# Kernel tuning notes

Measured on AMD Instinct MI355X. Metric: run time of the kernel, lower is better.

## Reference

```python
import jax, jax.numpy as jnp
import numpy as np

PI = 3.141592653589793
N = 4194304


def _lerp(a, b, w):
    return a + w * (b - a)


def _schlick(u):
    m = jnp.clip(1.0 - u, 0.0, 1.0)
    return m ** 5


def setup_inputs() -> dict:
    key = jax.random.key(0)
    kl, kv, kp = jax.random.split(key, 3)

    def unit_dirs(k):
        v = jax.random.normal(k, (N, 3), dtype=jnp.float32)
        v = v / jnp.linalg.norm(v, axis=-1, keepdims=True)
        # upper hemisphere so most samples pass the cos_nl/cos_nv >= 0 test
        return v.at[:, 2].set(jnp.abs(v[:, 2]))

    light = unit_dirs(kl)
    view = unit_dirs(kv)
    inputs = jnp.stack([light, view], axis=1)  # [N, 2, 3]

    return {
        "inputs": inputs,
        "base_color": jnp.array([0.8, 0.8, 0.8], dtype=jnp.float32),
        "metallic": jnp.array([0.3], dtype=jnp.float32),
        "subsurface": jnp.array([0.2], dtype=jnp.float32),
        "specular": jnp.array([0.5], dtype=jnp.float32),
        "roughness": jnp.array([0.5], dtype=jnp.float32),
        "specular_tint": jnp.array([0.1], dtype=jnp.float32),
        "anisotropic": jnp.array([0.2], dtype=jnp.float32),
        "sheen": jnp.array([0.3], dtype=jnp.float32),
        "sheen_tint": jnp.array([0.5], dtype=jnp.float32),
        "clear_coat": jnp.array([0.5], dtype=jnp.float32),
        "clear_coat_gloss": jnp.array([0.8], dtype=jnp.float32),
    }


def _brdf(inputs, base_color, metallic, subsurface, specular, roughness,
          specular_tint, anisotropic, sheen, sheen_tint, clear_coat,
          clear_coat_gloss):
    # scalar params
    mtl = metallic[0]; sub = subsurface[0]; spec = specular[0]
    rough = roughness[0]; sp_tint = specular_tint[0]; aniso = anisotropic[0]
    sh = sheen[0]; sh_tint = sheen_tint[0]; cc = clear_coat[0]
    cc_gloss = clear_coat_gloss[0]

    light = inputs[:, 0, :]  # [N, 3]
    view = inputs[:, 1, :]   # [N, 3]
    hv = light + view
    half = hv / jnp.linalg.norm(hv, axis=-1, keepdims=True)

    # tangent x=[1,0,0], bitangent y=[0,1,0], normal=[0,0,1]
    cos_nl = light[:, 2]
    cos_nv = view[:, 2]
    cos_nh = half[:, 2]
    cos_hl = jnp.sum(half * light, axis=-1)

    valid = (cos_nl >= 0) & (cos_nv >= 0)
    # grad-safe cosines for invalid (masked-out) samples
    cnl = jnp.where(valid, cos_nl, 0.5)
    cnv = jnp.where(valid, cos_nv, 0.5)

    cd_lin = base_color ** 2.2  # mon2lin
    cd_lum = 0.3 * cd_lin[0] + 0.6 * cd_lin[1] + 0.1 * cd_lin[2]
    c_tint = jnp.where(cd_lum > 0, cd_lin / jnp.maximum(cd_lum, 1e-20),
                       jnp.zeros(3, cd_lin.dtype))

    c_spec0 = _lerp(spec * 0.08 * _lerp(1.0, c_tint, sp_tint), cd_lin, mtl)  # [3]
    c_sheen = _lerp(1.0, c_tint, sh_tint)  # [3]

    fl = _schlick(cnl)
    fv = _schlick(cnv)
    fd90 = 0.5 + 2.0 * cos_hl ** 2 * rough
    fd = _lerp(1.0, fd90, fl) * _lerp(1.0, fd90, fv)
    fss90 = cos_hl ** 2 * rough
    fss = _lerp(1.0, fss90, fl) * _lerp(1.0, fss90, fv)
    ss = 1.25 * (fss * (1.0 / (cnl + cnv) - 0.5) + 0.5)

    aspect = jnp.sqrt(1.0 - aniso * 0.9)
    ax = jnp.maximum(0.001, rough ** 2 / aspect)
    ay = jnp.maximum(0.001, rough ** 2 * aspect)

    # GTR2 anisotropic distribution
    Ds = 1.0 / (PI * ax * ay * ((half[:, 0] / ax) ** 2 +
                                (half[:, 1] / ay) ** 2 + cos_nh ** 2) ** 2)
    FH = _schlick(cos_hl)
    Fs = _lerp(c_spec0[None, :], 1.0, FH[:, None])  # [N, 3]

    def g_aniso(c, cx, cy):
        return 1.0 / (c + jnp.sqrt((cx * ax) ** 2 + (cy * ay) ** 2 + c ** 2))

    Gs = g_aniso(cnl, light[:, 0], light[:, 1]) * g_aniso(cnv, view[:, 0], view[:, 1])
    specular_term = (Gs * Ds)[:, None] * Fs

    Fsheen = FH[:, None] * sh * c_sheen[None, :]
    diffuse = ((1.0 / PI) * _lerp(fd, ss, sub)[:, None] * cd_lin[None, :] +
               Fsheen) * (1.0 - mtl)

    # clearcoat: GTR1 with a = lerp(0.1, 0.001, gloss)
    a_cc = _lerp(0.1, 0.001, cc_gloss)
    a2 = a_cc ** 2
    t = 1.0 + (a2 - 1.0) * cos_nh ** 2
    Dr = jnp.where(a_cc >= 1.0, 1.0 / PI, (a2 - 1.0) / (PI * jnp.log(a2) * t))

    def g025(c):
        a = 0.0625  # 0.25^2
        return 1.0 / (c + jnp.sqrt(a + c ** 2 - a * c ** 2))

    Gr = g025(cnl) * g025(cnv)
    Fr = _lerp(0.04, 1.0, FH)
    clear = 0.25 * cc * Gr * Fr * Dr

    out = diffuse + specular_term + clear[:, None]
    return jnp.where(valid[:, None], out, 0.0)


@jax.jit
def reference(inputs, base_color, metallic, subsurface, specular, roughness,
              specular_tint, anisotropic, sheen, sheen_tint, clear_coat,
              clear_coat_gloss):
    return _brdf(inputs, base_color, metallic, subsurface, specular, roughness,
                 specular_tint, anisotropic, sheen, sheen_tint, clear_coat,
                 clear_coat_gloss)
```

## Files before the change

### kernel.cpp

```cpp
#include <hip/hip_runtime.h>

#define PI_F 3.14159265358979323846f
#define THREADS 256
#define PTS_PER_BLOCK 512

__device__ __forceinline__ float rcpf_(float x){ return __builtin_amdgcn_rcpf(x); }
__device__ __forceinline__ float sqrtf_(float x){ return __builtin_amdgcn_sqrtf(x); }

__device__ __forceinline__ float schlick5(float u){
    float m = 1.0f - u;
    float m2 = m * m;
    return m2 * m2 * m;
}

__device__ __forceinline__ void compute_uniforms(
    const float* bc, float mtl, float sub, float spec, float rough,
    float sp_tint, float aniso, float sh, float sh_tint, float cc, float ccg,
    float* u)
{
    const float cd0 = __powf(bc[0], 2.2f);
    const float cd1 = __powf(bc[1], 2.2f);
    const float cd2 = __powf(bc[2], 2.2f);
    const float lum = 0.3f*cd0 + 0.6f*cd1 + 0.1f*cd2;
    const float il  = rcpf_(fmaxf(lum, 1e-20f));
    const float ct0 = (lum > 0.f) ? cd0*il : 0.f;
    const float ct1 = (lum > 0.f) ? cd1*il : 0.f;
    const float ct2 = (lum > 0.f) ? cd2*il : 0.f;

    const float s008 = spec * 0.08f;
    const float b0 = s008 * (1.f + sp_tint*(ct0 - 1.f));
    const float b1 = s008 * (1.f + sp_tint*(ct1 - 1.f));
    const float b2 = s008 * (1.f + sp_tint*(ct2 - 1.f));
    const float cs0_0 = b0 + mtl*(cd0 - b0);
    const float cs0_1 = b1 + mtl*(cd1 - b1);
    const float cs0_2 = b2 + mtl*(cd2 - b2);

    const float om = 1.f - mtl;
    const float invpi = 1.f / PI_F;

    const float aspect = sqrtf_(1.f - aniso*0.9f);
    const float r2 = rough * rough;
    const float ax = fmaxf(0.001f, r2 * rcpf_(aspect));
    const float ay = fmaxf(0.001f, r2 * aspect);

    const float a_cc = 0.1f + (0.001f - 0.1f)*ccg;
    const float a2 = a_cc * a_cc;
    float a2m1, k_dr;
    if (a_cc >= 1.0f) { a2m1 = 0.f; k_dr = invpi; }
    else              { a2m1 = a2 - 1.f; k_dr = (a2 - 1.f) * rcpf_(PI_F * __logf(a2)); }

    u[0] = rough;
    u[1] = sub;
    u[2] = ax*ax;
    u[3] = ay*ay;
    u[4] = rcpf_(ax*ax);
    u[5] = rcpf_(ay*ay);
    u[6] = rcpf_(PI_F * ax * ay);
    u[7] = a2m1;
    u[8] = k_dr;
    u[9] = 0.25f * cc;
    u[10] = cd0 * om * invpi;
    u[11] = cd1 * om * invpi;
    u[12] = cd2 * om * invpi;
    u[13] = sh * (1.f + sh_tint*(ct0 - 1.f)) * om;
    u[14] = sh * (1.f + sh_tint*(ct1 - 1.f)) * om;
    u[15] = sh * (1.f + sh_tint*(ct2 - 1.f)) * om;
    u[16] = cs0_0;
    u[17] = cs0_1;
    u[18] = cs0_2;
    u[19] = 1.f - cs0_0;
    u[20] = 1.f - cs0_1;
    u[21] = 1.f - cs0_2;
}

__global__ void setup_kernel(
    const float* __restrict__ bc, const float* __restrict__ metallic,
    const float* __restrict__ subsurface, const float* __restrict__ specular,
    const float* __restrict__ roughness, const float* __restrict__ specular_tint,
    const float* __restrict__ anisotropic, const float* __restrict__ sheen,
    const float* __restrict__ sheen_tint, const float* __restrict__ clear_coat,
    const float* __restrict__ clear_coat_gloss, float* __restrict__ ws)
{
    if (threadIdx.x == 0) {
        float u[22];
        compute_uniforms(bc, metallic[0], subsurface[0], specular[0], roughness[0],
                         specular_tint[0], anisotropic[0], sheen[0], sheen_tint[0],
                         clear_coat[0], clear_coat_gloss[0], u);
        #pragma unroll
        for (int i = 0; i < 22; ++i) ws[i] = u[i];
    }
}

__global__ __launch_bounds__(THREADS, 4) void brdf_kernel(
    const float* __restrict__ in,
    const float* __restrict__ uws,
    float* __restrict__ out,
    int npts)
{
    __shared__ float4 s_in4[PTS_PER_BLOCK * 6 / 4];
    __shared__ float2 s_out2[PTS_PER_BLOCK * 3 / 2];
    float* s_in = reinterpret_cast<float*>(s_in4);
    float* s_out = reinterpret_cast<float*>(s_out2);

    float U[22];
    #pragma unroll
    for (int i = 0; i < 22; ++i) U[i] = uws[i];
    const float rough   = U[0],  sub     = U[1];
    const float ax2     = U[2],  ay2     = U[3];
    const float inv_ax2 = U[4],  inv_ay2 = U[5];
    const float k_ds    = U[6],  a2m1    = U[7];
    const float k_dr    = U[8],  cc_q    = U[9];
    const float two_rough = 2.f * rough;

    const int j = threadIdx.x;
    const size_t blk = blockIdx.x;

    const size_t total_f4 = (size_t)npts * 6 / 4;
    const float4* gin = reinterpret_cast<const float4*>(in);
    const size_t f4_base = blk * (PTS_PER_BLOCK * 6 / 4);
    #pragma unroll
    for (int k = 0; k < 3; ++k) {
        size_t idx = f4_base + j + k * THREADS;
        if (idx < total_f4) s_in4[j + k * THREADS] = gin[idx];
    }
    __syncthreads();

    #pragma unroll
    for (int k = 0; k < 2; ++k) {
        const int p = j + k * THREADS;
        const float l0 = s_in[6*p+0], l1 = s_in[6*p+1], l2 = s_in[6*p+2];
        const float v0 = s_in[6*p+3], v1 = s_in[6*p+4], v2 = s_in[6*p+5];

        const float hvx = l0 + v0, hvy = l1 + v1, hvz = l2 + v2;
        const float n2 = hvx*hvx + hvy*hvy + hvz*hvz;
        const float chl = 0.5f * sqrtf_(n2);
        const float chl2 = 0.25f * n2;

        const bool valid = (l2 >= 0.f) && (v2 >= 0.f);
        const float cnl = valid ? l2 : 0.5f;
        const float cnv = valid ? v2 : 0.5f;

        const float fl = schlick5(cnl);
        const float fv = schlick5(cnv);
        const float FH = schlick5(chl);

        const float fd90m1  = two_rough * chl2 - 0.5f;
        const float fd  = (1.f + fd90m1*fl) * (1.f + fd90m1*fv);
        const float fss90m1 = rough * chl2 - 1.f;
        const float fss = (1.f + fss90m1*fl) * (1.f + fss90m1*fv);
        const float ss = 1.25f * (fss * (rcpf_(cnl + cnv) - 0.5f) + 0.5f);
        const float dw = fd + sub * (ss - fd);

        const float dtermu = hvx*hvx*inv_ax2 + hvy*hvy*inv_ay2 + hvz*hvz;
        const float denL = cnl + sqrtf_(l0*l0*ax2 + l1*l1*ay2 + cnl*cnl);
        const float denV = cnv + sqrtf_(v0*v0*ax2 + v1*v1*ay2 + cnv*cnv);
        const float GsDs = k_ds * (n2 * n2) * rcpf_(dtermu*dtermu * denL * denV);

        const float tden = n2 + a2m1 * (hvz*hvz);
        const float grL = cnl + sqrtf_(0.0625f + 0.9375f*cnl*cnl);
        const float grV = cnv + sqrtf_(0.0625f + 0.9375f*cnv*cnv);
        const float Fr = 0.04f + 0.96f * FH;
        const float clear = cc_q * Fr * k_dr * n2 * rcpf_(tden * grL * grV);

        float r0 = dw*U[10] + FH*U[13] + GsDs*(U[16] + FH*U[19]) + clear;
        float r1 = dw*U[11] + FH*U[14] + GsDs*(U[17] + FH*U[20]) + clear;
        float r2 = dw*U[12] + FH*U[15] + GsDs*(U[18] + FH*U[21]) + clear;

        s_out[3*p+0] = valid ? r0 : 0.f;
        s_out[3*p+1] = valid ? r1 : 0.f;
        s_out[3*p+2] = valid ? r2 : 0.f;
    }
    __syncthreads();

    const size_t total_f2 = (size_t)npts * 3 / 2;
    float2* gout = reinterpret_cast<float2*>(out);
    const size_t f2_base = blk * (PTS_PER_BLOCK * 3 / 2);
    #pragma unroll
    for (int k = 0; k < 3; ++k) {
        size_t idx = f2_base + j + k * THREADS;
        if (idx < total_f2) gout[idx] = s_out2[j + k * THREADS];
    }
}

extern "C" void kernel_launch(void* const* d_in, const int* in_sizes, int n_in,
                              void* d_out, int out_size, void* d_ws, size_t ws_size,
                              hipStream_t stream) {
    const float* in = (const float*)d_in[0];
    const int npts = in_sizes[0] / 6;
    const int grid = (npts + PTS_PER_BLOCK - 1) / PTS_PER_BLOCK;

    float* ws = (float*)d_ws;
    setup_kernel<<<1, 64, 0, stream>>>(
        (const float*)d_in[1], (const float*)d_in[2], (const float*)d_in[3],
        (const float*)d_in[4], (const float*)d_in[5], (const float*)d_in[6],
        (const float*)d_in[7], (const float*)d_in[8], (const float*)d_in[9],
        (const float*)d_in[10], (const float*)d_in[11], ws);

    brdf_kernel<<<grid, THREADS, 0, stream>>>(in, ws, (float*)d_out, npts);
}
```

Before: 181.7 us.

## Use persistent grid-stride blocks with register prefetch of next tile

Replaces one-block-per-tile launch with a capped persistent grid of 1536 blocks that loop over tiles. Each iteration issues global loads for the next tile into registers before computing the current tile, so load latency overlaps compute. This cuts block launch overhead and keeps memory requests in flight, but adds register pressure (12 extra floats) and may lower occupancy under the existing launch bounds.

Result: slower. 186.3 us (+2.5%).

```diff
diff --git a/kernel.cpp b/kernel.cpp
--- a/kernel.cpp
+++ b/kernel.cpp
@@ -3,6 +3,9 @@
 #define PI_F 3.14159265358979323846f
 #define THREADS 256
 #define PTS_PER_BLOCK 512
+#define F4_PER_TILE (PTS_PER_BLOCK * 6 / 4)
+#define F2_PER_TILE (PTS_PER_BLOCK * 3 / 2)
+#define PERSIST_BLOCKS 1536
 
 __device__ __forceinline__ float rcpf_(float x){ return __builtin_amdgcn_rcpf(x); }
 __device__ __forceinline__ float sqrtf_(float x){ return __builtin_amdgcn_sqrtf(x); }
@@ -95,10 +98,10 @@
     const float* __restrict__ in,
     const float* __restrict__ uws,
     float* __restrict__ out,
-    int npts)
+    int npts, int ntiles)
 {
-    __shared__ float4 s_in4[PTS_PER_BLOCK * 6 / 4];
-    __shared__ float2 s_out2[PTS_PER_BLOCK * 3 / 2];
+    __shared__ float4 s_in4[F4_PER_TILE];
+    __shared__ float2 s_out2[F2_PER_TILE];
     float* s_in = reinterpret_cast<float*>(s_in4);
     float* s_out = reinterpret_cast<float*>(s_out2);
 
@@ -113,72 +116,95 @@
     const float two_rough = 2.f * rough;
 
     const int j = threadIdx.x;
-    const size_t blk = blockIdx.x;
-
     const size_t total_f4 = (size_t)npts * 6 / 4;
+    const size_t total_f2 = (size_t)npts * 3 / 2;
     const float4* gin = reinterpret_cast<const float4*>(in);
-    const size_t f4_base = blk * (PTS_PER_BLOCK * 6 / 4);
-    #pragma unroll
-    for (int k = 0; k < 3; ++k) {
-        size_t idx = f4_base + j + k * THREADS;
-        if (idx < total_f4) s_in4[j + k * THREADS] = gin[idx];
+    float2* gout = reinterpret_cast<float2*>(out);
+
+    int tile = blockIdx.x;
+    if (tile >= ntiles) return;
+
+    float4 r0, r1, r2;
+    {
+        const size_t b = (size_t)tile * F4_PER_TILE + j;
+        r0 = (b           < total_f4) ? gin[b]           : make_float4(0,0,0,0);
+        r1 = (b + THREADS < total_f4) ? gin[b + THREADS] : make_float4(0,0,0,0);
+        r2 = (b + 2*THREADS < total_f4) ? gin[b + 2*THREADS] : make_float4(0,0,0,0);
     }
-    __syncthreads();
-
-    #pragma unroll
-    for (int k = 0; k < 2; ++k) {
-        const int p = j + k * THREADS;
-        const float l0 = s_in[6*p+0], l1 = s_in[6*p+1], l2 = s_in[6*p+2];
-        const float v0 = s_in[6*p+3], v1 = s_in[6*p+4], v2 = s_in[6*p+5];
-
-        const float hvx = l0 + v0, hvy = l1 + v1, hvz = l2 + v2;
-        const float n2 = hvx*hvx + hvy*hvy + hvz*hvz;
-        const float chl = 0.5f * sqrtf_(n2);
-        const float chl2 = 0.25f * n2;
-
-        const bool valid = (l2 >= 0.f) && (v2 >= 0.f);
-        const float cnl = valid ? l2 : 0.5f;
-        const float cnv = valid ? v2 : 0.5f;
-
-        const float fl = schlick5(cnl);
-        const float fv = schlick5(cnv);
-        const float FH = schlick5(chl);
-
-        const float fd90m1  = two_rough * chl2 - 0.5f;
-        const float fd  = (1.f + fd90m1*fl) * (1.f + fd90m1*fv);
-        const float fss90m1 = rough * chl2 - 1.f;
-        const float fss = (1.f + fss90m1*fl) * (1.f + fss90m1*fv);
-        const float ss = 1.25f * (fss * (rcpf_(cnl + cnv) - 0.5f) + 0.5f);
-        const float dw = fd + sub * (ss - fd);
-
-        const float dtermu = hvx*hvx*inv_ax2 + hvy*hvy*inv_ay2 + hvz*hvz;
-        const float denL = cnl + sqrtf_(l0*l0*ax2 + l1*l1*ay2 + cnl*cnl);
-        const float denV = cnv + sqrtf_(v0*v0*ax2 + v1*v1*ay2 + cnv*cnv);
-        const float GsDs = k_ds * (n2 * n2) * rcpf_(dtermu*dtermu * denL * denV);
-
-        const float tden = n2 + a2m1 * (hvz*hvz);
-        const float grL = cnl + sqrtf_(0.0625f + 0.9375f*cnl*cnl);
-        const float grV = cnv + sqrtf_(0.0625f + 0.9375f*cnv*cnv);
-        const float Fr = 0.04f + 0.96f * FH;
-        const float clear = cc_q * Fr * k_dr * n2 * rcpf_(tden * grL * grV);
-
-        float r0 = dw*U[10] + FH*U[13] + GsDs*(U[16] + FH*U[19]) + clear;
-        float r1 = dw*U[11] + FH*U[14] + GsDs*(U[17] + FH*U[20]) + clear;
-        float r2 = dw*U[12] + FH*U[15] + GsDs*(U[18] + FH*U[21]) + clear;
-
-        s_out[3*p+0] = valid ? r0 : 0.f;
-        s_out[3*p+1] = valid ? r1 : 0.f;
-        s_out[3*p+2] = valid ? r2 : 0.f;
-    }
-    __syncthreads();
-
-    const size_t total_f2 = (size_t)npts * 3 / 2;
-    float2* gout = reinterpret_cast<float2*>(out);
-    const size_t f2_base = blk * (PTS_PER_BLOCK * 3 / 2);
-    #pragma unroll
-    for (int k = 0; k < 3; ++k) {
-        size_t idx = f2_base + j + k * THREADS;
-        if (idx < total_f2) gout[idx] = s_out2[j + k * THREADS];
+
+    while (true) {
+        const int next = tile + gridDim.x;
+
+        float4 p0 = make_float4(0,0,0,0), p1 = p0, p2 = p0;
+        if (next < ntiles) {
+            const size_t b = (size_t)next * F4_PER_TILE + j;
+            if (b             < total_f4) p0 = gin[b];
+            if (b + THREADS   < total_f4) p1 = gin[b + THREADS];
+            if (b + 2*THREADS < total_f4) p2 = gin[b + 2*THREADS];
+        }
+
+        s_in4[j]             = r0;
+        s_in4[j + THREADS]   = r1;
+        s_in4[j + 2*THREADS] = r2;
+        __syncthreads();
+
+        #pragma unroll
+        for (int k = 0; k < 2; ++k) {
+            const int p = j + k * THREADS;
+            const float l0 = s_in[6*p+0], l1 = s_in[6*p+1], l2 = s_in[6*p+2];
+            const float v0 = s_in[6*p+3], v1 = s_in[6*p+4], v2 = s_in[6*p+5];
+
+            const float hvx = l0 + v0, hvy = l1 + v1, hvz = l2 + v2;
+            const float n2 = hvx*hvx + hvy*hvy + hvz*hvz;
+            const float chl = 0.5f * sqrtf_(n2);
+            const float chl2 = 0.25f * n2;
+
+            const bool valid = (l2 >= 0.f) && (v2 >= 0.f);
+            const float cnl = valid ? l2 : 0.5f;
+            const float cnv = valid ? v2 : 0.5f;
+
+            const float fl = schlick5(cnl);
+            const float fv = schlick5(cnv);
+            const float FH = schlick5(chl);
+
+            const float fd90m1  = two_rough * chl2 - 0.5f;
+            const float fd  = (1.f + fd90m1*fl) * (1.f + fd90m1*fv);
+            const float fss90m1 = rough * chl2 - 1.f;
+            const float fss = (1.f + fss90m1*fl) * (1.f + fss90m1*fv);
+            const float ss = 1.25f * (fss * (rcpf_(cnl + cnv) - 0.5f) + 0.5f);
+            const float dw = fd + sub * (ss - fd);
+
+            const float dtermu = hvx*hvx*inv_ax2 + hvy*hvy*inv_ay2 + hvz*hvz;
+            const float denL = cnl + sqrtf_(l0*l0*ax2 + l1*l1*ay2 + cnl*cnl);
+            const float denV = cnv + sqrtf_(v0*v0*ax2 + v1*v1*ay2 + cnv*cnv);
+            const float GsDs = k_ds * (n2 * n2) * rcpf_(dtermu*dtermu * denL * denV);
+
+            const float tden = n2 + a2m1 * (hvz*hvz);
+            const float grL = cnl + sqrtf_(0.0625f + 0.9375f*cnl*cnl);
+            const float grV = cnv + sqrtf_(0.0625f + 0.9375f*cnv*cnv);
+            const float Fr = 0.04f + 0.96f * FH;
+            const float clear = cc_q * Fr * k_dr * n2 * rcpf_(tden * grL * grV);
+
+            float r0c = dw*U[10] + FH*U[13] + GsDs*(U[16] + FH*U[19]) + clear;
+            float r1c = dw*U[11] + FH*U[14] + GsDs*(U[17] + FH*U[20]) + clear;
+            float r2c = dw*U[12] + FH*U[15] + GsDs*(U[18] + FH*U[21]) + clear;
+
+            s_out[3*p+0] = valid ? r0c : 0.f;
+            s_out[3*p+1] = valid ? r1c : 0.f;
+            s_out[3*p+2] = valid ? r2c : 0.f;
+        }
+        __syncthreads();
+
+        {
+            const size_t b = (size_t)tile * F2_PER_TILE + j;
+            if (b             < total_f2) gout[b]             = s_out2[j];
+            if (b + THREADS   < total_f2) gout[b + THREADS]   = s_out2[j + THREADS];
+            if (b + 2*THREADS < total_f2) gout[b + 2*THREADS] = s_out2[j + 2*THREADS];
+        }
+
+        if (next >= ntiles) break;
+        r0 = p0; r1 = p1; r2 = p2;
+        tile = next;
     }
 }
 
@@ -187,7 +213,8 @@
                               hipStream_t stream) {
     const float* in = (const float*)d_in[0];
     const int npts = in_sizes[0] / 6;
-    const int grid = (npts + PTS_PER_BLOCK - 1) / PTS_PER_BLOCK;
+    const int ntiles = (npts + PTS_PER_BLOCK - 1) / PTS_PER_BLOCK;
+    const int grid = ntiles < PERSIST_BLOCKS ? ntiles : PERSIST_BLOCKS;
 
     float* ws = (float*)d_ws;
     setup_kernel<<<1, 64, 0, stream>>>(
@@ -196,5 +223,5 @@
         (const float*)d_in[7], (const float*)d_in[8], (const float*)d_in[9],
         (const float*)d_in[10], (const float*)d_in[11], ws);
 
-    brdf_kernel<<<grid, THREADS, 0, stream>>>(in, ws, (float*)d_out, npts);
-}
+    brdf_kernel<<<grid, THREADS, 0, stream>>>(in, ws, (float*)d_out, npts, ntiles);
+}
```

## Convert BRDF kernel to persistent grid with four-deep register prefetch of tiles

Applied to the files above, without the earlier changes.

Launches a capped grid of persistent blocks that loop over tiles, keeping four tiles of input prefetched in registers while the current tile is staged through shared memory and computed. The goal is to overlap global loads with compute and cut block launch overhead. In exchange it uses many more registers per thread, which can lower occupancy, and the fixed block count may leave compute units unevenly loaded.

Measured after the change: 187.5 us. 3.2% more time.

```diff
diff --git a/kernel.cpp b/kernel.cpp
--- a/kernel.cpp
+++ b/kernel.cpp
@@ -3,6 +3,9 @@
 #define PI_F 3.14159265358979323846f
 #define THREADS 256
 #define PTS_PER_BLOCK 512
+#define F4T (PTS_PER_BLOCK * 6 / 4)
+#define F2T (PTS_PER_BLOCK * 3 / 2)
+#define PERSIST_BLOCKS 1024
 
 __device__ __forceinline__ float rcpf_(float x){ return __builtin_amdgcn_rcpf(x); }
 __device__ __forceinline__ float sqrtf_(float x){ return __builtin_amdgcn_sqrtf(x); }
@@ -95,10 +98,10 @@
     const float* __restrict__ in,
     const float* __restrict__ uws,
     float* __restrict__ out,
-    int npts)
+    int npts, int ntiles)
 {
-    __shared__ float4 s_in4[PTS_PER_BLOCK * 6 / 4];
-    __shared__ float2 s_out2[PTS_PER_BLOCK * 3 / 2];
+    __shared__ float4 s_in4[F4T];
+    __shared__ float2 s_out2[F2T];
     float* s_in = reinterpret_cast<float*>(s_in4);
     float* s_out = reinterpret_cast<float*>(s_out2);
 
@@ -113,73 +116,98 @@
     const float two_rough = 2.f * rough;
 
     const int j = threadIdx.x;
-    const size_t blk = blockIdx.x;
-
+    const int gs = gridDim.x;
     const size_t total_f4 = (size_t)npts * 6 / 4;
+    const size_t total_f2 = (size_t)npts * 3 / 2;
     const float4* gin = reinterpret_cast<const float4*>(in);
-    const size_t f4_base = blk * (PTS_PER_BLOCK * 6 / 4);
-    #pragma unroll
-    for (int k = 0; k < 3; ++k) {
-        size_t idx = f4_base + j + k * THREADS;
-        if (idx < total_f4) s_in4[j + k * THREADS] = gin[idx];
+    float2* gout = reinterpret_cast<float2*>(out);
+
+    int t = blockIdx.x;
+    if (t >= ntiles) return;
+
+    float4 A0,A1,A2, B0,B1,B2, C0,C1,C2, D0,D1,D2;
+
+#define LOADT(tt, Ra, Rb, Rc) do {                                        \
+        Ra = Rb = Rc = make_float4(0.f,0.f,0.f,0.f);                      \
+        if ((tt) < ntiles) {                                              \
+            const size_t _b = (size_t)(tt) * F4T + j;                     \
+            if (_b               < total_f4) Ra = gin[_b];                \
+            if (_b +   THREADS   < total_f4) Rb = gin[_b + THREADS];      \
+            if (_b + 2*THREADS   < total_f4) Rc = gin[_b + 2*THREADS];    \
+        }                                                                 \
+    } while (0)
+
+    LOADT(t,        A0, A1, A2);
+    LOADT(t +   gs, B0, B1, B2);
+    LOADT(t + 2*gs, C0, C1, C2);
+    LOADT(t + 3*gs, D0, D1, D2);
+
+#define STEP(Ra, Rb, Rc) do {                                             \
+           \
+        s_in4[j]             = Ra;                                        \
+        s_in4[j + THREADS]   = Rb;                                        \
+        s_in4[j + 2*THREADS] = Rc;                                        \
+             \
+        LOADT(t + 4*gs, Ra, Rb, Rc);                                      \
+        __syncthreads();                                                  \
+        _Pragma("unroll")                                                 \
+        for (int k = 0; k < 2; ++k) {                                     \
+            const int p = j + k * THREADS;                                \
+            const float l0 = s_in[6*p+0], l1 = s_in[6*p+1], l2 = s_in[6*p+2]; \
+            const float v0 = s_in[6*p+3], v1 = s_in[6*p+4], v2 = s_in[6*p+5]; \
+            const float hvx = l0 + v0, hvy = l1 + v1, hvz = l2 + v2;      \
+            const float n2 = hvx*hvx + hvy*hvy + hvz*hvz;                 \
+            const float chl = 0.5f * sqrtf_(n2);                          \
+            const float chl2 = 0.25f * n2;                                \
+            const bool valid = (l2 >= 0.f) && (v2 >= 0.f);                \
+            const float cnl = valid ? l2 : 0.5f;                          \
+            const float cnv = valid ? v2 : 0.5f;                          \
+            const float fl = schlick5(cnl);                               \
+            const float fv = schlick5(cnv);                               \
+            const float FH = schlick5(chl);                               \
+            const float fd90m1  = two_rough * chl2 - 0.5f;                \
+            const float fd  = (1.f + fd90m1*fl) * (1.f + fd90m1*fv);      \
+            const float fss90m1 = rough * chl2 - 1.f;                     \
+            const float fss = (1.f + fss90m1*fl) * (1.f + fss90m1*fv);    \
+            const float ss = 1.25f * (fss * (rcpf_(cnl + cnv) - 0.5f) + 0.5f); \
+            const float dw = fd + sub * (ss - fd);                        \
+            const float dtermu = hvx*hvx*inv_ax2 + hvy*hvy*inv_ay2 + hvz*hvz; \
+            const float denL = cnl + sqrtf_(l0*l0*ax2 + l1*l1*ay2 + cnl*cnl); \
+            const float denV = cnv + sqrtf_(v0*v0*ax2 + v1*v1*ay2 + cnv*cnv); \
+            const float GsDs = k_ds * (n2 * n2) * rcpf_(dtermu*dtermu * denL * denV); \
+            const float tden = n2 + a2m1 * (hvz*hvz);                     \
+            const float grL = cnl + sqrtf_(0.0625f + 0.9375f*cnl*cnl);    \
+            const float grV = cnv + sqrtf_(0.0625f + 0.9375f*cnv*cnv);    \
+            const float Fr = 0.04f + 0.96f * FH;                          \
+            const float clear = cc_q * Fr * k_dr * n2 * rcpf_(tden * grL * grV); \
+            float r0c = dw*U[10] + FH*U[13] + GsDs*(U[16] + FH*U[19]) + clear; \
+            float r1c = dw*U[11] + FH*U[14] + GsDs*(U[17] + FH*U[20]) + clear; \
+            float r2c = dw*U[12] + FH*U[15] + GsDs*(U[18] + FH*U[21]) + clear; \
+            s_out[3*p+0] = valid ? r0c : 0.f;                             \
+            s_out[3*p+1] = valid ? r1c : 0.f;                             \
+            s_out[3*p+2] = valid ? r2c : 0.f;                             \
+        }                                                                 \
+        __syncthreads();                                                  \
+        {                                                                 \
+            const size_t _b = (size_t)t * F2T + j;                        \
+            if (_b               < total_f2) gout[_b]               = s_out2[j]; \
+            if (_b +   THREADS   < total_f2) gout[_b +   THREADS]   = s_out2[j + THREADS]; \
+            if (_b + 2*THREADS   < total_f2) gout[_b + 2*THREADS]   = s_out2[j + 2*THREADS]; \
+        }                                                                 \
+        t += gs;                                                          \
+    } while (0)
+
+    while (t < ntiles) {
+        STEP(A0, A1, A2);
+        if (t >= ntiles) break;
+        STEP(B0, B1, B2);
+        if (t >= ntiles) break;
+        STEP(C0, C1, C2);
+        if (t >= ntiles) break;
+        STEP(D0, D1, D2);
     }
-    __syncthreads();
-
-    #pragma unroll
-    for (int k = 0; k < 2; ++k) {
-        const int p = j + k * THREADS;
-        const float l0 = s_in[6*p+0], l1 = s_in[6*p+1], l2 = s_in[6*p+2];
-        const float v0 = s_in[6*p+3], v1 = s_in[6*p+4], v2 = s_in[6*p+5];
-
-        const float hvx = l0 + v0, hvy = l1 + v1, hvz = l2 + v2;
-        const float n2 = hvx*hvx + hvy*hvy + hvz*hvz;
-        const float chl = 0.5f * sqrtf_(n2);
-        const float chl2 = 0.25f * n2;
-
-        const bool valid = (l2 >= 0.f) && (v2 >= 0.f);
-        const float cnl = valid ? l2 : 0.5f;
-        const float cnv = valid ? v2 : 0.5f;
-
-        const float fl = schlick5(cnl);
-        const float fv = schlick5(cnv);
-        const float FH = schlick5(chl);
-
-        const float fd90m1  = two_rough * chl2 - 0.5f;
-        const float fd  = (1.f + fd90m1*fl) * (1.f + fd90m1*fv);
-        const float fss90m1 = rough * chl2 - 1.f;
-        const float fss = (1.f + fss90m1*fl) * (1.f + fss90m1*fv);
-        const float ss = 1.25f * (fss * (rcpf_(cnl + cnv) - 0.5f) + 0.5f);
-        const float dw = fd + sub * (ss - fd);
-
-        const float dtermu = hvx*hvx*inv_ax2 + hvy*hvy*inv_ay2 + hvz*hvz;
-        const float denL = cnl + sqrtf_(l0*l0*ax2 + l1*l1*ay2 + cnl*cnl);
-        const float denV = cnv + sqrtf_(v0*v0*ax2 + v1*v1*ay2 + cnv*cnv);
-        const float GsDs = k_ds * (n2 * n2) * rcpf_(dtermu*dtermu * denL * denV);
-
-        const float tden = n2 + a2m1 * (hvz*hvz);
-        const float grL = cnl + sqrtf_(0.0625f + 0.9375f*cnl*cnl);
-        const float grV = cnv + sqrtf_(0.0625f + 0.9375f*cnv*cnv);
-        const float Fr = 0.04f + 0.96f * FH;
-        const float clear = cc_q * Fr * k_dr * n2 * rcpf_(tden * grL * grV);
-
-        float r0 = dw*U[10] + FH*U[13] + GsDs*(U[16] + FH*U[19]) + clear;
-        float r1 = dw*U[11] + FH*U[14] + GsDs*(U[17] + FH*U[20]) + clear;
-        float r2 = dw*U[12] + FH*U[15] + GsDs*(U[18] + FH*U[21]) + clear;
-
-        s_out[3*p+0] = valid ? r0 : 0.f;
-        s_out[3*p+1] = valid ? r1 : 0.f;
-        s_out[3*p+2] = valid ? r2 : 0.f;
-    }
-    __syncthreads();
-
-    const size_t total_f2 = (size_t)npts * 3 / 2;
-    float2* gout = reinterpret_cast<float2*>(out);
-    const size_t f2_base = blk * (PTS_PER_BLOCK * 3 / 2);
-    #pragma unroll
-    for (int k = 0; k < 3; ++k) {
-        size_t idx = f2_base + j + k * THREADS;
-        if (idx < total_f2) gout[idx] = s_out2[j + k * THREADS];
-    }
+#undef STEP
+#undef LOADT
 }
 
 extern "C" void kernel_launch(void* const* d_in, const int* in_sizes, int n_in,
@@ -187,7 +215,8 @@
                               hipStream_t stream) {
     const float* in = (const float*)d_in[0];
     const int npts = in_sizes[0] / 6;
-    const int grid = (npts + PTS_PER_BLOCK - 1) / PTS_PER_BLOCK;
+    const int ntiles = (npts + PTS_PER_BLOCK - 1) / PTS_PER_BLOCK;
+    const int grid = ntiles < PERSIST_BLOCKS ? ntiles : PERSIST_BLOCKS;
 
     float* ws = (float*)d_ws;
     setup_kernel<<<1, 64, 0, stream>>>(
@@ -196,5 +225,5 @@
         (const float*)d_in[7], (const float*)d_in[8], (const float*)d_in[9],
         (const float*)d_in[10], (const float*)d_in[11], ws);
 
-    brdf_kernel<<<grid, THREADS, 0, stream>>>(in, ws, (float*)d_out, npts);
-}
+    brdf_kernel<<<grid, THREADS, 0, stream>>>(in, ws, (float*)d_out, npts, ntiles);
+}
```
